# Kernel tuning notes

Measured on AMD Instinct MI355X. Metric: run time of the kernel, lower is better.

## Reference

```python
import jax, jax.numpy as jnp
import numpy as np

M, K, N = 2048, 4096, 11008
Q_ABS_MAX = 128.0  # x_scaled_abs_max_fp for w8a8
Q_MIN, Q_MAX = -128, 127


def setup_inputs() -> dict:
    key = jax.random.key(0)
    k1, k2, k3, k4 = jax.random.split(key, 4)
    x = jax.random.normal(k1, (M, K), dtype=jnp.float32)
    # pre-quantized int8 weight, stored [K, N] (transposed layout as in quantize_weights)
    w_q = jax.random.randint(k2, (K, N), Q_MIN, Q_MAX + 1, dtype=jnp.int32).astype(jnp.int8)
    bias = jax.random.normal(k3, (N,), dtype=jnp.float32) * 0.01
    # per-tensor weight dequant scale (q_scale of the quantized weight)
    y_scale = jax.random.uniform(k4, (1,), dtype=jnp.float32, minval=0.001, maxval=0.02)
    return {"x": x, "w_q": w_q, "bias": bias, "y_scale": y_scale}


def reference(x, w_q, bias, y_scale):
    # dynamic per-tensor activation quantization: scale = max|x| / 128
    x_scale = jnp.max(jnp.abs(x)) / jnp.float32(Q_ABS_MAX)
    x_q = jnp.clip(jnp.round(x / x_scale), Q_MIN, Q_MAX).astype(jnp.int8)
    c = jnp.matmul(x_q.astype(jnp.int32), w_q.astype(jnp.int32))
    # dequantize + bias
    y = c.astype(jnp.float32) * (x_scale * y_scale[0]) + bias
    return y
```

## Files before the change

### kernel.cpp

```cpp
#include <hip/hip_runtime.h>
#include <stdint.h>

#define M_DIM 2048
#define K_DIM 4096
#define N_DIM 11008

typedef int v4i  __attribute__((ext_vector_type(4)));
typedef int v16i __attribute__((ext_vector_type(16)));

#define WS_XQ_OFF   65536ull
#define WS_WT_OFF   8454144ull
#define WS_FULL_BYTES (8454144ull + 45088768ull)
#define WS_SMALL_BYTES 8454144ull

static __device__ __forceinline__ void llds16(const void* g, void* l) {
  __builtin_amdgcn_global_load_lds(
      reinterpret_cast<const uint32_t __attribute__((address_space(1)))*>(
          reinterpret_cast<uintptr_t>(g)),
      reinterpret_cast<uint32_t __attribute__((address_space(3)))*>(
          reinterpret_cast<uintptr_t>(l)),
      16, 0, 0);
}

__global__ __launch_bounds__(256) void absmax_kernel(const float* __restrict__ x,
                                                     float* __restrict__ part) {
  __shared__ float red[256];
  const int g = blockIdx.x * 256 + threadIdx.x;
  const float4* x4 = reinterpret_cast<const float4*>(x);
  float m = 0.f;
#pragma unroll
  for (int i = 0; i < 8; ++i) {
    float4 v = x4[(size_t)i * 262144 + g];
    m = fmaxf(m, fmaxf(fmaxf(fabsf(v.x), fabsf(v.y)),
                       fmaxf(fabsf(v.z), fabsf(v.w))));
  }
  red[threadIdx.x] = m;
  __syncthreads();
  for (int s = 128; s > 0; s >>= 1) {
    if (threadIdx.x < s) red[threadIdx.x] = fmaxf(red[threadIdx.x], red[threadIdx.x + s]);
    __syncthreads();
  }
  if (threadIdx.x == 0) part[blockIdx.x] = red[0];
}

__global__ __launch_bounds__(256) void finalize_scale(const float* __restrict__ part,
                                                      const float* __restrict__ y_scale,
                                                      float* __restrict__ scales) {
  __shared__ float red[256];
  const int t = threadIdx.x;
  float m = fmaxf(fmaxf(part[t], part[t + 256]), fmaxf(part[t + 512], part[t + 768]));
  red[t] = m;
  __syncthreads();
  for (int s = 128; s > 0; s >>= 1) {
    if (t < s) red[t] = fmaxf(red[t], red[t + s]);
    __syncthreads();
  }
  if (t == 0) {
    float xs = red[0] * (1.0f / 128.0f);
    scales[0] = xs;
    scales[1] = xs * y_scale[0];
  }
}

static __device__ __forceinline__ int quant4(float4 v, float s) {
  int q0 = (int)rintf(v.x / s);
  int q1 = (int)rintf(v.y / s);
  int q2 = (int)rintf(v.z / s);
  int q3 = (int)rintf(v.w / s);
  q0 = max(-128, min(127, q0));
  q1 = max(-128, min(127, q1));
  q2 = max(-128, min(127, q2));
  q3 = max(-128, min(127, q3));
  return (q0 & 255) | ((q1 & 255) << 8) | ((q2 & 255) << 16) | ((q3 & 255) << 24);
}

__global__ __launch_bounds__(256) void quant_pack(const float* __restrict__ x,
                                                  const float* __restrict__ scales,
                                                  signed char* __restrict__ xq) {
  const float s = scales[0];
  const int g = blockIdx.x * 256 + threadIdx.x;
  const int mblk = g >> 15;
  const int kt = (g >> 9) & 63;
  const int u = g & 511;
  const int row = mblk * 128 + ((u >> 7) & 3) * 32 + (u & 31);
  const int kf = kt * 64 + ((u >> 6) & 1) * 32 + ((u >> 5) & 1) * 16;
  const float4* xp = reinterpret_cast<const float4*>(x + (size_t)row * K_DIM + kf);
  v4i o;
#pragma unroll
  for (int i = 0; i < 4; ++i) o[i] = quant4(xp[i], s);
  *reinterpret_cast<v4i*>(xq + (size_t)g * 16) = o;
}

__global__ __launch_bounds__(256) void quant_rowmajor(const float* __restrict__ x,
                                                      const float* __restrict__ scales,
                                                      signed char* __restrict__ xq) {
  const float s = scales[0];
  const size_t t = (size_t)blockIdx.x * 256 + threadIdx.x;
  const float4* x4 = reinterpret_cast<const float4*>(x) + t * 4;
  v4i o;
#pragma unroll
  for (int i = 0; i < 4; ++i) o[i] = quant4(x4[i], s);
  *reinterpret_cast<v4i*>(xq + t * 16) = o;
}

__global__ __launch_bounds__(256) void transpose_pack(const int* __restrict__ w,
                                                      signed char* __restrict__ wt) {
  __shared__ int tile[64 * 65];
  const int t = threadIdx.x;
  const int bx = blockIdx.x;
  const int by = blockIdx.y;
  const int n0 = bx * 64;
  const int k0 = by * 64;
#pragma unroll
  for (int p = 0; p < 4; ++p) {
    const int id = p * 256 + t;
    const int r = id >> 4;
    const int c4 = id & 15;
    v4i v = *reinterpret_cast<const v4i*>(w + (size_t)(k0 + r) * N_DIM + n0 + c4 * 4);
    tile[r * 65 + c4 * 4 + 0] = v[0];
    tile[r * 65 + c4 * 4 + 1] = v[1];
    tile[r * 65 + c4 * 4 + 2] = v[2];
    tile[r * 65 + c4 * 4 + 3] = v[3];
  }
  __syncthreads();
  const int nl = ((t >> 7) << 5) | (t & 31);
  const int kc = (t >> 5) & 3;
  v4i o;
#pragma unroll
  for (int q = 0; q < 4; ++q) {
    const int kb = kc * 16 + q * 4;
    int b0 = tile[(kb + 0) * 65 + nl] & 255;
    int b1 = tile[(kb + 1) * 65 + nl] & 255;
    int b2 = tile[(kb + 2) * 65 + nl] & 255;
    int b3 = tile[(kb + 3) * 65 + nl] & 255;
    o[q] = b0 | (b1 << 8) | (b2 << 16) | (b3 << 24);
  }
  const size_t base = ((size_t)(bx >> 2) * 64 + by) * 16384;
  const int ubase = ((bx & 3) * 2) << 7;
  *reinterpret_cast<v4i*>(wt + base + (size_t)(ubase + t) * 16) = o;
}

#define V8_TILE_B 24576
#define V8_NT     (K_DIM / 64)

__global__ __launch_bounds__(512, 4) void gemm_i8_v8(
    const signed char* __restrict__ xq, const signed char* __restrict__ wt,
    const float* __restrict__ scales, const float* __restrict__ bias,
    float* __restrict__ y) {
  __shared__ __align__(16) signed char smem[3 * V8_TILE_B];
  const int tid = threadIdx.x;

  const int bid = blockIdx.x;
  const int swz = (bid & 7) * 86 + (bid >> 3);
  const int mblk = swz & 15;
  const int nblk = swz >> 4;
  const int m0 = mblk * 128;
  const int n0 = nblk * 256;

  const signed char* gA = xq + (size_t)mblk * 64 * 8192;
  const signed char* gB = wt + (size_t)nblk * 64 * 16384;
  signed char* const ld = smem + tid * 16;

#define STAGE(kt, soff)                                                   \
  do {                                                                    \
    llds16(gA + (size_t)(kt) * 8192 + tid * 16,         ld + (soff));     \
    llds16(gB + (size_t)(kt) * 16384 + tid * 16,        ld + (soff) + 8192);  \
    llds16(gB + (size_t)(kt) * 16384 + 8192 + tid * 16, ld + (soff) + 16384); \
  } while (0)

  const int lane = tid & 63;
  const int wid = tid >> 6;
  const int wm = wid >> 2;
  const int wn = wid & 3;
  const int aoff = (wm * 2) * 2048 + lane * 16;
  const int boff = 8192 + (wn * 2) * 2048 + lane * 16;

  v16i acc[2][2] = {};

#define COMPUTE(roff)                                                         \
  do {                                                                        \
    const signed char* bp_ = smem + (roff);                                   \
    _Pragma("unroll")                                                         \
    for (int ks_ = 0; ks_ < 2; ++ks_) {                                       \
      v4i a0 = *reinterpret_cast<const v4i*>(bp_ + aoff + ks_ * 1024);        \
      v4i a1 = *reinterpret_cast<const v4i*>(bp_ + aoff + 2048 + ks_ * 1024); \
      v4i b0 = *reinterpret_cast<const v4i*>(bp_ + boff + ks_ * 1024);        \
      v4i b1 = *reinterpret_cast<const v4i*>(bp_ + boff + 2048 + ks_ * 1024); \
      acc[0][0] = __builtin_amdgcn_mfma_i32_32x32x32_i8(a0, b0, acc[0][0], 0, 0, 0); \
      acc[0][1] = __builtin_amdgcn_mfma_i32_32x32x32_i8(a0, b1, acc[0][1], 0, 0, 0); \
      acc[1][0] = __builtin_amdgcn_mfma_i32_32x32x32_i8(a1, b0, acc[1][0], 0, 0, 0); \
      acc[1][1] = __builtin_amdgcn_mfma_i32_32x32x32_i8(a1, b1, acc[1][1], 0, 0, 0); \
    }                                                                         \
  } while (0)

  STAGE(0, 0);
  STAGE(1, V8_TILE_B);
  asm volatile("s_waitcnt vmcnt(3)" ::: "memory");
  __builtin_amdgcn_s_barrier();

  int rOff = 0;
  int sOff = 2 * V8_TILE_B;
  for (int t = 0; t < V8_NT - 2; ++t) {
    STAGE(t + 2, sOff);
    COMPUTE(rOff);
    asm volatile("s_waitcnt vmcnt(3)" ::: "memory");
    __builtin_amdgcn_s_barrier();
    rOff = (rOff == 2 * V8_TILE_B) ? 0 : rOff + V8_TILE_B;
    sOff = (sOff == 2 * V8_TILE_B) ? 0 : sOff + V8_TILE_B;
  }
  COMPUTE(rOff);
  asm volatile("s_waitcnt vmcnt(0)" ::: "memory");
  __builtin_amdgcn_s_barrier();
  rOff = (rOff == 2 * V8_TILE_B) ? 0 : rOff + V8_TILE_B;
  COMPUTE(rOff);

#undef STAGE
#undef COMPUTE

  const float s = scales[1];
  const int l31 = lane & 31;
  const int lh4 = (lane >> 5) * 4;
#pragma unroll
  for (int fb = 0; fb < 2; ++fb) {
    const int col = n0 + wn * 64 + fb * 32 + l31;
    const float bv = bias[col];
#pragma unroll
    for (int fa = 0; fa < 2; ++fa) {
      const int rbase = m0 + wm * 64 + fa * 32 + lh4;
#pragma unroll
      for (int reg = 0; reg < 16; ++reg) {
        const int row = rbase + (reg & 3) + 8 * (reg >> 2);
        y[(size_t)row * N_DIM + col] = (float)acc[fa][fb][reg] * s + bv;
      }
    }
  }
}

#if defined(__has_builtin)
#if __has_builtin(__builtin_amdgcn_sdot4)
#define HAVE_SDOT4 1
#endif
#endif

static __device__ __forceinline__ int dot4(int a, int b, int c) {
#ifdef HAVE_SDOT4
  return __builtin_amdgcn_sdot4(a, b, c, false);
#else
  c += (int)(signed char)(a) * (int)(signed char)(b);
  c += (int)(signed char)(a >> 8) * (int)(signed char)(b >> 8);
  c += (int)(signed char)(a >> 16) * (int)(signed char)(b >> 16);
  c += (int)(signed char)(a >> 24) * (int)(signed char)(b >> 24);
  return c;
#endif
}

__global__ __launch_bounds__(256) void gemm_fallback(
    const signed char* __restrict__ xq, const int* __restrict__ w,
    const float* __restrict__ scales, const float* __restrict__ bias,
    float* __restrict__ y) {
  __shared__ int lds_a[64 * 17];
  __shared__ int lds_b[64 * 17];
  const int t = threadIdx.x;
  const int m0 = blockIdx.y * 64;
  const int n0 = blockIdx.x * 64;
  const int my = (t >> 4) * 4;
  const int nx = (t & 15) * 4;
  int acc[4][4] = {};
  for (int kt = 0; kt < K_DIM / 64; ++kt) {
    const int k0 = kt * 64;
    {
      const int r = t >> 2, sg = t & 3;
      v4i v = *reinterpret_cast<const v4i*>(xq + (size_t)(m0 + r) * K_DIM + k0 + sg * 16);
      lds_a[r * 17 + sg * 4 + 0] = v[0];
      lds_a[r * 17 + sg * 4 + 1] = v[1];
      lds_a[r * 17 + sg * 4 + 2] = v[2];
      lds_a[r * 17 + sg * 4 + 3] = v[3];
    }
    {
      const int n = t & 63, bkk = (t >> 6) * 4;
#pragma unroll
      for (int q = 0; q < 4; ++q) {
        const int kk = bkk + q;
        int b0 = w[(size_t)(k0 + kk * 4 + 0) * N_DIM + n0 + n] & 255;
        int b1 = w[(size_t)(k0 + kk * 4 + 1) * N_DIM + n0 + n] & 255;
        int b2 = w[(size_t)(k0 + kk * 4 + 2) * N_DIM + n0 + n] & 255;
        int b3 = w[(size_t)(k0 + kk * 4 + 3) * N_DIM + n0 + n] & 255;
        lds_b[n * 17 + kk] = b0 | (b1 << 8) | (b2 << 16) | (b3 << 24);
      }
    }
    __syncthreads();
#pragma unroll
    for (int kk = 0; kk < 16; ++kk) {
      int a[4], b[4];
#pragma unroll
      for (int i = 0; i < 4; ++i) a[i] = lds_a[(my + i) * 17 + kk];
#pragma unroll
      for (int j = 0; j < 4; ++j) b[j] = lds_b[(nx + j) * 17 + kk];
#pragma unroll
      for (int i = 0; i < 4; ++i)
#pragma unroll
        for (int j = 0; j < 4; ++j) acc[i][j] = dot4(a[i], b[j], acc[i][j]);
    }
    __syncthreads();
  }
  const float s = scales[1];
#pragma unroll
  for (int i = 0; i < 4; ++i)
#pragma unroll
    for (int j = 0; j < 4; ++j)
      y[(size_t)(m0 + my + i) * N_DIM + n0 + nx + j] =
          (float)acc[i][j] * s + bias[n0 + nx + j];
}

extern "C" void kernel_launch(void* const* d_in, const int* in_sizes, int n_in,
                              void* d_out, int out_size, void* d_ws, size_t ws_size,
                              hipStream_t stream) {
  (void)in_sizes; (void)n_in; (void)out_size;
  const float* x = (const float*)d_in[0];
  const int* w = (const int*)d_in[1];
  const float* bias = (const float*)d_in[2];
  const float* yscale = (const float*)d_in[3];
  float* y = (float*)d_out;
  char* ws = (char*)d_ws;
  float* scales = (float*)(ws);
  float* part = (float*)(ws + 1024);
  signed char* xq = (signed char*)(ws + WS_XQ_OFF);
  signed char* wt = (signed char*)(ws + WS_WT_OFF);

  if (ws_size < WS_SMALL_BYTES) return;

  absmax_kernel<<<1024, 256, 0, stream>>>(x, part);
  finalize_scale<<<1, 256, 0, stream>>>(part, yscale, scales);
  if (ws_size >= WS_FULL_BYTES) {
    quant_pack<<<2048, 256, 0, stream>>>(x, scales, xq);
    transpose_pack<<<dim3(N_DIM / 64, K_DIM / 64), 256, 0, stream>>>(w, wt);
    gemm_i8_v8<<<(M_DIM / 128) * (N_DIM / 256), 512, 0, stream>>>(xq, wt, scales, bias, y);
  } else {
    quant_rowmajor<<<2048, 256, 0, stream>>>(x, scales, xq);
    gemm_fallback<<<dim3(N_DIM / 64, M_DIM / 64), 256, 0, stream>>>(xq, w, scales, bias, y);
  }
}
```

Measured before the change: 158.9 us.

## Halve GEMM block to 4 waves with 64x128 per-wave output tiles

The int8 GEMM block drops from 512 to 256 threads (2x2 waves). Each wave now computes a 64x128 output tile with 8 MFMA accumulators instead of 4, and the global-to-LDS staging is split into six loads per thread. This raises MFMA work per LDS read of the A fragments and cuts the wave count per tile, aiming to lower LDS traffic and overhead. The cost is about twice the accumulator registers per wave, which may reduce occupancy, and fewer waves left to hide load latency.

```diff
diff --git a/kernel.cpp b/kernel.cpp
--- a/kernel.cpp
+++ b/kernel.cpp
@@ -140,14 +140,14 @@
   *reinterpret_cast<v4i*>(wt + base + (size_t)(ubase + t) * 16) = o;
 }
 
-#define V8_TILE_B 24576
-#define V8_NT     (K_DIM / 64)
-
-__global__ __launch_bounds__(512, 4) void gemm_i8_v8(
+#define V9_TILE_B 24576
+#define V9_NT     (K_DIM / 64)
+
+__global__ __launch_bounds__(256, 2) void gemm_i8_v9(
     const signed char* __restrict__ xq, const signed char* __restrict__ wt,
     const float* __restrict__ scales, const float* __restrict__ bias,
     float* __restrict__ y) {
-  __shared__ __align__(16) signed char smem[3 * V8_TILE_B];
+  __shared__ __align__(16) signed char smem[3 * V9_TILE_B];
   const int tid = threadIdx.x;
 
   const int bid = blockIdx.x;
@@ -161,57 +161,68 @@
   const signed char* gB = wt + (size_t)nblk * 64 * 16384;
   signed char* const ld = smem + tid * 16;
 
-#define STAGE(kt, soff)                                                   \
-  do {                                                                    \
-    llds16(gA + (size_t)(kt) * 8192 + tid * 16,         ld + (soff));     \
-    llds16(gB + (size_t)(kt) * 16384 + tid * 16,        ld + (soff) + 8192);  \
-    llds16(gB + (size_t)(kt) * 16384 + 8192 + tid * 16, ld + (soff) + 16384); \
+#define STAGE(kt, soff)                                                       \
+  do {                                                                        \
+    const size_t a_ = (size_t)(kt) * 8192 + tid * 16;                         \
+    const size_t b_ = (size_t)(kt) * 16384 + tid * 16;                        \
+    llds16(gA + a_,         ld + (soff));                                     \
+    llds16(gA + a_ + 4096,  ld + (soff) + 4096);                              \
+    llds16(gB + b_,         ld + (soff) + 8192);                              \
+    llds16(gB + b_ + 4096,  ld + (soff) + 12288);                             \
+    llds16(gB + b_ + 8192,  ld + (soff) + 16384);                             \
+    llds16(gB + b_ + 12288, ld + (soff) + 20480);                             \
   } while (0)
 
   const int lane = tid & 63;
   const int wid = tid >> 6;
-  const int wm = wid >> 2;
-  const int wn = wid & 3;
+  const int wm = wid >> 1;
+  const int wn = wid & 1;
   const int aoff = (wm * 2) * 2048 + lane * 16;
-  const int boff = 8192 + (wn * 2) * 2048 + lane * 16;
-
-  v16i acc[2][2] = {};
-
-#define COMPUTE(roff)                                                         \
-  do {                                                                        \
-    const signed char* bp_ = smem + (roff);                                   \
-    _Pragma("unroll")                                                         \
-    for (int ks_ = 0; ks_ < 2; ++ks_) {                                       \
-      v4i a0 = *reinterpret_cast<const v4i*>(bp_ + aoff + ks_ * 1024);        \
-      v4i a1 = *reinterpret_cast<const v4i*>(bp_ + aoff + 2048 + ks_ * 1024); \
-      v4i b0 = *reinterpret_cast<const v4i*>(bp_ + boff + ks_ * 1024);        \
-      v4i b1 = *reinterpret_cast<const v4i*>(bp_ + boff + 2048 + ks_ * 1024); \
+  const int boff = 8192 + (wn * 4) * 2048 + lane * 16;
+
+  v16i acc[2][4] = {};
+
+#define COMPUTE(roff)                                                          \
+  do {                                                                         \
+    const signed char* bp_ = smem + (roff);                                    \
+    _Pragma("unroll")                                                          \
+    for (int ks_ = 0; ks_ < 2; ++ks_) {                                        \
+      v4i a0 = *reinterpret_cast<const v4i*>(bp_ + aoff + ks_ * 1024);         \
+      v4i a1 = *reinterpret_cast<const v4i*>(bp_ + aoff + 2048 + ks_ * 1024);  \
+      v4i b0 = *reinterpret_cast<const v4i*>(bp_ + boff + ks_ * 1024);         \
+      v4i b1 = *reinterpret_cast<const v4i*>(bp_ + boff + 2048 + ks_ * 1024);  \
+      v4i b2 = *reinterpret_cast<const v4i*>(bp_ + boff + 4096 + ks_ * 1024);  \
+      v4i b3 = *reinterpret_cast<const v4i*>(bp_ + boff + 6144 + ks_ * 1024);  \
       acc[0][0] = __builtin_amdgcn_mfma_i32_32x32x32_i8(a0, b0, acc[0][0], 0, 0, 0); \
       acc[0][1] = __builtin_amdgcn_mfma_i32_32x32x32_i8(a0, b1, acc[0][1], 0, 0, 0); \
+      acc[0][2] = __builtin_amdgcn_mfma_i32_32x32x32_i8(a0, b2, acc[0][2], 0, 0, 0); \
+      acc[0][3] = __builtin_amdgcn_mfma_i32_32x32x32_i8(a0, b3, acc[0][3], 0, 0, 0); \
       acc[1][0] = __builtin_amdgcn_mfma_i32_32x32x32_i8(a1, b0, acc[1][0], 0, 0, 0); \
       acc[1][1] = __builtin_amdgcn_mfma_i32_32x32x32_i8(a1, b1, acc[1][1], 0, 0, 0); \
-    }                                                                         \
+      acc[1][2] = __builtin_amdgcn_mfma_i32_32x32x32_i8(a1, b2, acc[1][2], 0, 0, 0); \
+      acc[1][3] = __builtin_amdgcn_mfma_i32_32x32x32_i8(a1, b3, acc[1][3], 0, 0, 0); \
+    }                                                                          \
   } while (0)
 
   STAGE(0, 0);
-  STAGE(1, V8_TILE_B);
-  asm volatile("s_waitcnt vmcnt(3)" ::: "memory");
+  STAGE(1, V9_TILE_B);
+  asm volatile("s_waitcnt vmcnt(6)" ::: "memory");
   __builtin_amdgcn_s_barrier();
 
   int rOff = 0;
-  int sOff = 2 * V8_TILE_B;
-  for (int t = 0; t < V8_NT - 2; ++t) {
+  int sOff = 2 * V9_TILE_B;
+  for (int t = 0; t < V9_NT - 2; ++t) {
     STAGE(t + 2, sOff);
     COMPUTE(rOff);
-    asm volatile("s_waitcnt vmcnt(3)" ::: "memory");
+    asm volatile("s_waitcnt vmcnt(6)" ::: "memory");
     __builtin_amdgcn_s_barrier();
-    rOff = (rOff == 2 * V8_TILE_B) ? 0 : rOff + V8_TILE_B;
-    sOff = (sOff == 2 * V8_TILE_B) ? 0 : sOff + V8_TILE_B;
+    rOff = (rOff == 2 * V9_TILE_B) ? 0 : rOff + V9_TILE_B;
+    sOff = (sOff == 2 * V9_TILE_B) ? 0 : sOff + V9_TILE_B;
   }
   COMPUTE(rOff);
   asm volatile("s_waitcnt vmcnt(0)" ::: "memory");
   __builtin_amdgcn_s_barrier();
-  rOff = (rOff == 2 * V8_TILE_B) ? 0 : rOff + V8_TILE_B;
+  rOff = (rOff == 2 * V9_TILE_B) ? 0 : rOff + V9_TILE_B;
   COMPUTE(rOff);
 
 #undef STAGE
@@ -221,8 +232,8 @@
   const int l31 = lane & 31;
   const int lh4 = (lane >> 5) * 4;
 #pragma unroll
-  for (int fb = 0; fb < 2; ++fb) {
-    const int col = n0 + wn * 64 + fb * 32 + l31;
+  for (int fb = 0; fb < 4; ++fb) {
+    const int col = n0 + wn * 128 + fb * 32 + l31;
     const float bv = bias[col];
 #pragma unroll
     for (int fa = 0; fa < 2; ++fa) {
@@ -334,7 +345,7 @@
   if (ws_size >= WS_FULL_BYTES) {
     quant_pack<<<2048, 256, 0, stream>>>(x, scales, xq);
     transpose_pack<<<dim3(N_DIM / 64, K_DIM / 64), 256, 0, stream>>>(w, wt);
-    gemm_i8_v8<<<(M_DIM / 128) * (N_DIM / 256), 512, 0, stream>>>(xq, wt, scales, bias, y);
+    gemm_i8_v9<<<(M_DIM / 128) * (N_DIM / 256), 256, 0, stream>>>(xq, wt, scales, bias, y);
   } else {
     quant_rowmajor<<<2048, 256, 0, stream>>>(x, scales, xq);
     gemm_fallback<<<dim3(N_DIM / 64, M_DIM / 64), 256, 0, stream>>>(xq, w, scales, bias, y);
```

New measurement: 160.9 us. About the same (+1.2%).

## Replace LDS-staged GEMM with register double-buffered direct global loads

Applied to the files above, without the earlier changes.

Rewrites the int8 GEMM so each wave loads its MFMA operand fragments straight from global memory into registers, double-buffered across K steps, instead of staging tiles in LDS with a three-buffer ring and barriers. The block tile becomes 256x128 with 4 waves each computing 64x128, which drops all LDS traffic and block-level synchronization. The trade-off is much higher register pressure from 8 accumulators plus two sets of 12 operand registers. Operand tiles are no longer shared through LDS, so each wave fetches its own A and B fragments and relies on the caches for reuse.

```diff
diff --git a/kernel.cpp b/kernel.cpp
--- a/kernel.cpp
+++ b/kernel.cpp
@@ -140,93 +140,93 @@
   *reinterpret_cast<v4i*>(wt + base + (size_t)(ubase + t) * 16) = o;
 }
 
-#define V8_TILE_B 24576
-#define V8_NT     (K_DIM / 64)
-
-__global__ __launch_bounds__(512, 4) void gemm_i8_v8(
+__global__ __launch_bounds__(256, 2) void gemm_i8_v11(
     const signed char* __restrict__ xq, const signed char* __restrict__ wt,
     const float* __restrict__ scales, const float* __restrict__ bias,
     float* __restrict__ y) {
-  __shared__ __align__(16) signed char smem[3 * V8_TILE_B];
   const int tid = threadIdx.x;
+  const int lane = tid & 63;
+  const int w = tid >> 6;
 
   const int bid = blockIdx.x;
   const int swz = (bid & 7) * 86 + (bid >> 3);
-  const int mblk = swz & 15;
-  const int nblk = swz >> 4;
-  const int m0 = mblk * 128;
-  const int n0 = nblk * 256;
-
-  const signed char* gA = xq + (size_t)mblk * 64 * 8192;
-  const signed char* gB = wt + (size_t)nblk * 64 * 16384;
-  signed char* const ld = smem + tid * 16;
-
-#define STAGE(kt, soff)                                                   \
-  do {                                                                    \
-    llds16(gA + (size_t)(kt) * 8192 + tid * 16,         ld + (soff));     \
-    llds16(gB + (size_t)(kt) * 16384 + tid * 16,        ld + (soff) + 8192);  \
-    llds16(gB + (size_t)(kt) * 16384 + 8192 + tid * 16, ld + (soff) + 16384); \
+  const int bm = swz & 7;
+  const int bn = swz >> 3;
+
+  const int amblk = bm * 2 + (w >> 1);
+  const int agrp0 = (w & 1) * 2;
+  const signed char* gA = xq + (size_t)amblk * 64 * 8192 + agrp0 * 2048 + lane * 16;
+  const signed char* gB = wt + (size_t)(bn >> 1) * 64 * 16384 + (bn & 1) * 4 * 2048
+                             + lane * 16;
+
+#define LOADK(kt, A0, A1, A2, A3, B0, B1, B2, B3, B4, B5, B6, B7)              \
+  do {                                                                         \
+    const signed char* pa_ = gA + (size_t)(kt) * 8192;                         \
+    const signed char* pb_ = gB + (size_t)(kt) * 16384;                        \
+    A0 = *reinterpret_cast<const v4i*>(pa_);                      \
+    A1 = *reinterpret_cast<const v4i*>(pa_ + 1024);               \
+    A2 = *reinterpret_cast<const v4i*>(pa_ + 2048);               \
+    A3 = *reinterpret_cast<const v4i*>(pa_ + 3072);               \
+    B0 = *reinterpret_cast<const v4i*>(pb_);                                   \
+    B1 = *reinterpret_cast<const v4i*>(pb_ + 1024);                            \
+    B2 = *reinterpret_cast<const v4i*>(pb_ + 2048);                            \
+    B3 = *reinterpret_cast<const v4i*>(pb_ + 3072);                            \
+    B4 = *reinterpret_cast<const v4i*>(pb_ + 4096);                            \
+    B5 = *reinterpret_cast<const v4i*>(pb_ + 5120);                            \
+    B6 = *reinterpret_cast<const v4i*>(pb_ + 6144);                            \
+    B7 = *reinterpret_cast<const v4i*>(pb_ + 7168);                            \
   } while (0)
 
-  const int lane = tid & 63;
-  const int wid = tid >> 6;
-  const int wm = wid >> 2;
-  const int wn = wid & 3;
-  const int aoff = (wm * 2) * 2048 + lane * 16;
-  const int boff = 8192 + (wn * 2) * 2048 + lane * 16;
-
-  v16i acc[2][2] = {};
-
-#define COMPUTE(roff)                                                         \
-  do {                                                                        \
-    const signed char* bp_ = smem + (roff);                                   \
-    _Pragma("unroll")                                                         \
-    for (int ks_ = 0; ks_ < 2; ++ks_) {                                       \
-      v4i a0 = *reinterpret_cast<const v4i*>(bp_ + aoff + ks_ * 1024);        \
-      v4i a1 = *reinterpret_cast<const v4i*>(bp_ + aoff + 2048 + ks_ * 1024); \
-      v4i b0 = *reinterpret_cast<const v4i*>(bp_ + boff + ks_ * 1024);        \
-      v4i b1 = *reinterpret_cast<const v4i*>(bp_ + boff + 2048 + ks_ * 1024); \
-      acc[0][0] = __builtin_amdgcn_mfma_i32_32x32x32_i8(a0, b0, acc[0][0], 0, 0, 0); \
-      acc[0][1] = __builtin_amdgcn_mfma_i32_32x32x32_i8(a0, b1, acc[0][1], 0, 0, 0); \
-      acc[1][0] = __builtin_amdgcn_mfma_i32_32x32x32_i8(a1, b0, acc[1][0], 0, 0, 0); \
-      acc[1][1] = __builtin_amdgcn_mfma_i32_32x32x32_i8(a1, b1, acc[1][1], 0, 0, 0); \
-    }                                                                         \
+#define COMPK(A0, A1, A2, A3, B0, B1, B2, B3, B4, B5, B6, B7)                  \
+  do {                                                                         \
+    acc[0][0] = __builtin_amdgcn_mfma_i32_32x32x32_i8(A0, B0, acc[0][0], 0, 0, 0); \
+    acc[0][1] = __builtin_amdgcn_mfma_i32_32x32x32_i8(A0, B2, acc[0][1], 0, 0, 0); \
+    acc[0][2] = __builtin_amdgcn_mfma_i32_32x32x32_i8(A0, B4, acc[0][2], 0, 0, 0); \
+    acc[0][3] = __builtin_amdgcn_mfma_i32_32x32x32_i8(A0, B6, acc[0][3], 0, 0, 0); \
+    acc[1][0] = __builtin_amdgcn_mfma_i32_32x32x32_i8(A2, B0, acc[1][0], 0, 0, 0); \
+    acc[1][1] = __builtin_amdgcn_mfma_i32_32x32x32_i8(A2, B2, acc[1][1], 0, 0, 0); \
+    acc[1][2] = __builtin_amdgcn_mfma_i32_32x32x32_i8(A2, B4, acc[1][2], 0, 0, 0); \
+    acc[1][3] = __builtin_amdgcn_mfma_i32_32x32x32_i8(A2, B6, acc[1][3], 0, 0, 0); \
+    acc[0][0] = __builtin_amdgcn_mfma_i32_32x32x32_i8(A1, B1, acc[0][0], 0, 0, 0); \
+    acc[0][1] = __builtin_amdgcn_mfma_i32_32x32x32_i8(A1, B3, acc[0][1], 0, 0, 0); \
+    acc[0][2] = __builtin_amdgcn_mfma_i32_32x32x32_i8(A1, B5, acc[0][2], 0, 0, 0); \
+    acc[0][3] = __builtin_amdgcn_mfma_i32_32x32x32_i8(A1, B7, acc[0][3], 0, 0, 0); \
+    acc[1][0] = __builtin_amdgcn_mfma_i32_32x32x32_i8(A3, B1, acc[1][0], 0, 0, 0); \
+    acc[1][1] = __builtin_amdgcn_mfma_i32_32x32x32_i8(A3, B3, acc[1][1], 0, 0, 0); \
+    acc[1][2] = __builtin_amdgcn_mfma_i32_32x32x32_i8(A3, B5, acc[1][2], 0, 0, 0); \
+    acc[1][3] = __builtin_amdgcn_mfma_i32_32x32x32_i8(A3, B7, acc[1][3], 0, 0, 0); \
   } while (0)
 
-  STAGE(0, 0);
-  STAGE(1, V8_TILE_B);
-  asm volatile("s_waitcnt vmcnt(3)" ::: "memory");
-  __builtin_amdgcn_s_barrier();
-
-  int rOff = 0;
-  int sOff = 2 * V8_TILE_B;
-  for (int t = 0; t < V8_NT - 2; ++t) {
-    STAGE(t + 2, sOff);
-    COMPUTE(rOff);
-    asm volatile("s_waitcnt vmcnt(3)" ::: "memory");
-    __builtin_amdgcn_s_barrier();
-    rOff = (rOff == 2 * V8_TILE_B) ? 0 : rOff + V8_TILE_B;
-    sOff = (sOff == 2 * V8_TILE_B) ? 0 : sOff + V8_TILE_B;
-  }
-  COMPUTE(rOff);
-  asm volatile("s_waitcnt vmcnt(0)" ::: "memory");
-  __builtin_amdgcn_s_barrier();
-  rOff = (rOff == 2 * V8_TILE_B) ? 0 : rOff + V8_TILE_B;
-  COMPUTE(rOff);
-
-#undef STAGE
-#undef COMPUTE
+  v16i acc[2][4] = {};
+  v4i xa0, xa1, xa2, xa3, xb0, xb1, xb2, xb3, xb4, xb5, xb6, xb7;
+  v4i ya0, ya1, ya2, ya3, yb0, yb1, yb2, yb3, yb4, yb5, yb6, yb7;
+
+  LOADK(0, xa0, xa1, xa2, xa3, xb0, xb1, xb2, xb3, xb4, xb5, xb6, xb7);
+  for (int t = 0; t < 62; t += 2) {
+    LOADK(t + 1, ya0, ya1, ya2, ya3, yb0, yb1, yb2, yb3, yb4, yb5, yb6, yb7);
+    COMPK(xa0, xa1, xa2, xa3, xb0, xb1, xb2, xb3, xb4, xb5, xb6, xb7);
+    LOADK(t + 2, xa0, xa1, xa2, xa3, xb0, xb1, xb2, xb3, xb4, xb5, xb6, xb7);
+    COMPK(ya0, ya1, ya2, ya3, yb0, yb1, yb2, yb3, yb4, yb5, yb6, yb7);
+  }
+  LOADK(63, ya0, ya1, ya2, ya3, yb0, yb1, yb2, yb3, yb4, yb5, yb6, yb7);
+  COMPK(xa0, xa1, xa2, xa3, xb0, xb1, xb2, xb3, xb4, xb5, xb6, xb7);
+  COMPK(ya0, ya1, ya2, ya3, yb0, yb1, yb2, yb3, yb4, yb5, yb6, yb7);
+
+#undef LOADK
+#undef COMPK
 
   const float s = scales[1];
   const int l31 = lane & 31;
   const int lh4 = (lane >> 5) * 4;
-#pragma unroll
-  for (int fb = 0; fb < 2; ++fb) {
-    const int col = n0 + wn * 64 + fb * 32 + l31;
+  const int row0 = bm * 256 + w * 64;
+  const int col0 = bn * 128;
+#pragma unroll
+  for (int fb = 0; fb < 4; ++fb) {
+    const int col = col0 + fb * 32 + l31;
     const float bv = bias[col];
 #pragma unroll
     for (int fa = 0; fa < 2; ++fa) {
-      const int rbase = m0 + wm * 64 + fa * 32 + lh4;
+      const int rbase = row0 + fa * 32 + lh4;
 #pragma unroll
       for (int reg = 0; reg < 16; ++reg) {
         const int row = rbase + (reg & 3) + 8 * (reg >> 2);
@@ -334,7 +334,7 @@
   if (ws_size >= WS_FULL_BYTES) {
     quant_pack<<<2048, 256, 0, stream>>>(x, scales, xq);
     transpose_pack<<<dim3(N_DIM / 64, K_DIM / 64), 256, 0, stream>>>(w, wt);
-    gemm_i8_v8<<<(M_DIM / 128) * (N_DIM / 256), 512, 0, stream>>>(xq, wt, scales, bias, y);
+    gemm_i8_v11<<<688, 256, 0, stream>>>(xq, wt, scales, bias, y);
   } else {
     quant_rowmajor<<<2048, 256, 0, stream>>>(x, scales, xq);
     gemm_fallback<<<dim3(N_DIM / 64, M_DIM / 64), 256, 0, stream>>>(xq, w, scales, bias, y);
```

Result: slower. 185.5 us (+16.7%).
